# Kernel optimization log

Measured on AMD Instinct MI355X. Metric: run time of the kernel, lower is better.

Reference implementation:

```python
import jax, jax.numpy as jnp
import numpy as np

EPS = 1e-8
B, L, D = 8, 2048, 128

def _l2norm(x):
    # F.normalize-style: x / max(||x||, eps)
    n = jnp.sqrt(jnp.sum(x * x, axis=-1, keepdims=True))
    return x / jnp.maximum(n, EPS)

def setup_inputs() -> dict:
    key = jax.random.key(0)
    k0, k1, k2, k3, k4 = jax.random.split(key, 5)
    context = jax.random.normal(k0, (B, 2, L, D), dtype=jnp.float32)
    # MlpModule (BLINK-style): Linear(D, D) -> ReLU -> Linear(D, 1)
    W1 = jax.random.normal(k1, (D, D), dtype=jnp.float32) * (1.0 / np.sqrt(D))
    b1 = jnp.zeros((D,), dtype=jnp.float32)
    W2 = jax.random.normal(k2, (D, 1), dtype=jnp.float32) * (1.0 / np.sqrt(D))
    b2 = jnp.zeros((1,), dtype=jnp.float32)
    return {"context": context, "W1": W1, "b1": b1, "W2": W2, "b2": b2}

def reference(context, W1, b1, W2, b2):
    ctx = context[:, 0]          # [B, L, D] mention-side tokens
    ent = context[:, 1]          # [B, L, D] entity-side tokens
    cn = _l2norm(ctx)
    en = _l2norm(ent)
    # cosine similarity matrix [B, L, L]
    sim = jnp.einsum("bld,bmd->blm", cn, en)
    idx = jnp.argmax(sim, axis=-1)                          # [B, L]
    matched = jnp.take_along_axis(en, idx[..., None], axis=1)  # [B, L, D]
    pair = jnp.stack([cn, matched], axis=-2)                # [B, L, 2, D]
    h = jax.nn.relu(pair @ W1 + b1)                         # [B, L, 2, D]
    out = h @ W2 + b2                                       # [B, L, 2, 1]
    return jnp.sum(out, axis=-2).squeeze(-1)                # [B, L]
```

## Files before the change

### kernel.cpp

```cpp
#include <hip/hip_runtime.h>
#include <hip/hip_bf16.h>

#define B_ 8
#define L_ 2048
#define D_ 128
#define BL_ (B_ * L_)
#define DELTA2 0.016f
#define QCAP 4096

typedef __attribute__((ext_vector_type(8))) short bf16x8;
typedef __attribute__((ext_vector_type(4))) float f32x4;

__device__ __forceinline__ void gload_lds16(const void* g, void* l) {
    __builtin_amdgcn_global_load_lds(
        (const __attribute__((address_space(1))) unsigned int*)g,
        (__attribute__((address_space(3))) unsigned int*)l, 16, 0, 0);
}

#define WAIT_VM(N) asm volatile("s_waitcnt vmcnt(" #N ")" ::: "memory")

__global__ void k_norm(const float* __restrict__ ctx,
                       float* __restrict__ cn, float* __restrict__ en,
                       ushort* __restrict__ cnb, ushort* __restrict__ enb) {
    int wid  = blockIdx.x * 4 + (threadIdx.x >> 6);
    int lane = threadIdx.x & 63;
    int b   = wid >> 12;
    int rem = wid & 4095;
    int c   = rem >> 11;
    int l   = rem & 2047;

    const float* src = ctx + (size_t)wid * D_;
    float2 v = ((const float2*)src)[lane];
    float ss = v.x * v.x + v.y * v.y;
    #pragma unroll
    for (int off = 32; off; off >>= 1) ss += __shfl_down(ss, off, 64);
    ss = __shfl(ss, 0, 64);
    float n = fmaxf(sqrtf(ss), 1e-8f);
    float ox = v.x / n, oy = v.y / n;

    size_t ro = (size_t)(b * L_ + l) * D_;
    float* dst = (c == 0 ? cn : en) + ro;
    ((float2*)dst)[lane] = make_float2(ox, oy);

    __hip_bfloat16 hx = __float2bfloat16(ox), hy = __float2bfloat16(oy);
    ushort ux = *(ushort*)&hx, uy = *(ushort*)&hy;
    ushort* dstb = (c == 0 ? cnb : enb) + ro;
    ((ushort2*)dstb)[lane] = make_ushort2(ux, uy);
}

__global__ __launch_bounds__(512, 2) void k_sim(const ushort* __restrict__ cnb,
                                                const ushort* __restrict__ enb,
                                                const float* __restrict__ cn,
                                                const float* __restrict__ en,
                                                int* __restrict__ finalidx) {
    __shared__ __align__(16) char Bsm[8][4][4096];
    __shared__ float wrowmax[8][64];
    __shared__ float rowth_l[64];
    __shared__ unsigned long long best[64];
    __shared__ int qbuf[QCAP];
    __shared__ int qn;

    const int bid = blockIdx.x;
    const int b = bid & 7, rb = bid >> 3;
    const int row0 = rb * 64;
    const int tid = threadIdx.x;
    const int wave = tid >> 6, lane = tid & 63;
    const int m = lane & 15, q = lane >> 4;

    if (tid == 0) qn = 0;
    if (tid < 64) best[tid] = 0ULL;

    const ushort* Ab = cnb + ((size_t)(b * L_) + row0) * D_;
    const char* gw = (const char*)(enb + (size_t)(b * L_) * D_) + (size_t)wave * 65536;
    char* Bw = &Bsm[wave][0][0];

    bf16x8 Areg[16];
    #pragma unroll
    for (int rt = 0; rt < 4; ++rt)
        #pragma unroll
        for (int kc = 0; kc < 4; ++kc)
            Areg[rt * 4 + kc] = *(const bf16x8*)(Ab + (size_t)(rt * 16 + m) * D_ + kc * 32 + q * 8);

    auto STAGE = [&](int c) {
        const char* gc = gw + (size_t)c * 4096;
        char* lbuf = Bw + (c & 3) * 4096;
        #pragma unroll
        for (int i = 0; i < 4; ++i) {
            int j = i * 4 + q;
            int so = j * 256 + ((m ^ (j & 7)) << 4);
            gload_lds16(gc + so, lbuf + i * 1024);
        }
    };
    auto TILE = [&](int c, f32x4 acc[4]) {
        const char* lbuf = Bw + (c & 3) * 4096;
        #pragma unroll
        for (int rt = 0; rt < 4; ++rt) acc[rt] = (f32x4){0.f, 0.f, 0.f, 0.f};
        #pragma unroll
        for (int kc = 0; kc < 4; ++kc) {
            bf16x8 bf = *(const bf16x8*)(lbuf + m * 256 + ((kc * 64 + q * 16) ^ ((m & 7) << 4)));
            #pragma unroll
            for (int rt = 0; rt < 4; ++rt)
                acc[rt] = __builtin_amdgcn_mfma_f32_16x16x32_bf16(Areg[rt * 4 + kc], bf, acc[rt], 0, 0, 0);
        }
    };

    float runmax[16];
    #pragma unroll
    for (int s = 0; s < 16; ++s) runmax[s] = -3.0e38f;

    auto FMAX = [&](const f32x4 acc[4]) {
        #pragma unroll
        for (int rt = 0; rt < 4; ++rt)
            #pragma unroll
            for (int reg = 0; reg < 4; ++reg)
                runmax[rt * 4 + reg] = fmaxf(runmax[rt * 4 + reg], acc[rt][reg]);
    };

    STAGE(0); STAGE(1); STAGE(2);
    #pragma unroll 1
    for (int c = 0; c < 14; ++c) {
        WAIT_VM(8);
        f32x4 acc[4];
        TILE(c, acc);
        if (c < 13) STAGE(c + 3);
        FMAX(acc);
    }
    { WAIT_VM(4); f32x4 acc[4]; TILE(14, acc); FMAX(acc); }
    { WAIT_VM(0); f32x4 acc[4]; TILE(15, acc); FMAX(acc); }

    #pragma unroll
    for (int s = 0; s < 16; ++s) {
        float v = runmax[s];
        v = fmaxf(v, __shfl_xor(v, 1, 64));
        v = fmaxf(v, __shfl_xor(v, 2, 64));
        v = fmaxf(v, __shfl_xor(v, 4, 64));
        v = fmaxf(v, __shfl_xor(v, 8, 64));
        runmax[s] = v;
    }
    if (m == 0) {
        #pragma unroll
        for (int rt = 0; rt < 4; ++rt)
            #pragma unroll
            for (int reg = 0; reg < 4; ++reg)
                wrowmax[wave][rt * 16 + q * 4 + reg] = runmax[rt * 4 + reg];
    }
    __syncthreads();
    if (tid < 64) {
        float rm = wrowmax[0][tid];
        #pragma unroll
        for (int w = 1; w < 8; ++w) rm = fmaxf(rm, wrowmax[w][tid]);
        rowth_l[tid] = rm - DELTA2;
    }
    __syncthreads();
    float rowth_r[16];
    #pragma unroll
    for (int rt = 0; rt < 4; ++rt)
        #pragma unroll
        for (int reg = 0; reg < 4; ++reg)
            rowth_r[rt * 4 + reg] = rowth_l[rt * 16 + q * 4 + reg];

    auto CAPT = [&](int c, const f32x4 acc[4]) {
        int col = wave * 256 + c * 16 + m;
        #pragma unroll
        for (int rt = 0; rt < 4; ++rt)
            #pragma unroll
            for (int reg = 0; reg < 4; ++reg)
                if (acc[rt][reg] >= rowth_r[rt * 4 + reg]) {
                    int row = rt * 16 + q * 4 + reg;
                    int pos = atomicAdd(&qn, 1);
                    if (pos < QCAP) qbuf[pos] = (row << 12) | col;
                }
    };

    #pragma unroll 1
    for (int d = 0; d < 4; ++d) {
        f32x4 acc[4];
        TILE(15 - d, acc);
        STAGE(11 - d);
        CAPT(15 - d, acc);
    }
    #pragma unroll 1
    for (int d = 4; d < 13; ++d) {
        WAIT_VM(12);
        f32x4 acc[4];
        TILE(15 - d, acc);
        if (d < 12) STAGE(11 - d);
        CAPT(15 - d, acc);
    }
    { WAIT_VM(8); f32x4 acc[4]; TILE(2, acc); CAPT(2, acc); }
    { WAIT_VM(4); f32x4 acc[4]; TILE(1, acc); CAPT(1, acc); }
    { WAIT_VM(0); f32x4 acc[4]; TILE(0, acc); CAPT(0, acc); }
    __syncthreads();

    int qtot = min(qn, QCAP);
    for (int e0 = wave * 4; e0 < qtot; e0 += 32) {
        int e = e0 + q;
        bool act = (e < qtot);
        int pc = qbuf[act ? e : (qtot - 1)];
        int rl = (pc >> 12) & 63, col = pc & 0xFFF;
        const float* ar = cn + ((size_t)(b * L_) + row0 + rl) * D_;
        const float* br = en + ((size_t)(b * L_) + col) * D_;
        float4 x0 = ((const float4*)ar)[m * 2], x1 = ((const float4*)ar)[m * 2 + 1];
        float4 y0 = ((const float4*)br)[m * 2], y1 = ((const float4*)br)[m * 2 + 1];
        double s = (double)x0.x * y0.x + (double)x0.y * y0.y +
                   (double)x0.z * y0.z + (double)x0.w * y0.w +
                   (double)x1.x * y1.x + (double)x1.y * y1.y +
                   (double)x1.z * y1.z + (double)x1.w * y1.w;
        s += __shfl_xor(s, 1, 64);
        s += __shfl_xor(s, 2, 64);
        s += __shfl_xor(s, 4, 64);
        s += __shfl_xor(s, 8, 64);
        if (act && m == 0) {
            unsigned long long ub = (unsigned long long)__double_as_longlong(s);
            ub = (ub & 0x8000000000000000ULL) ? ~ub : (ub | 0x8000000000000000ULL);
            ub = (ub & ~0x7FFULL) | (unsigned long long)(2047 - col);
            atomicMax(&best[rl], ub);
        }
    }
    __syncthreads();
    if (tid < 64)
        finalidx[b * L_ + row0 + tid] = 2047 - (int)(best[tid] & 0x7FFULL);
}

__global__ __launch_bounds__(512) void k_mlp(
        const float* __restrict__ cn, const float* __restrict__ en,
        const int* __restrict__ finalidx,
        const float* __restrict__ W1, const float* __restrict__ b1,
        const float* __restrict__ W2, const float* __restrict__ b2,
        float* __restrict__ out) {
    __shared__ __align__(16) float As[32][68];
    __shared__ __align__(16) float Bs[32][132];
    __shared__ float redv[2][32][16];
    __shared__ int fidxs[32];

    int tid = threadIdx.x;
    int tx = tid & 15, ty = tid >> 4;
    int rr = tid >> 3, kg = tid & 7;
    int R0 = blockIdx.x * 32;
    int b  = R0 >> 11;
    int l0 = R0 & 2047;

    if (tid < 32) fidxs[tid] = finalidx[R0 + tid];

    const float* cnr = cn + ((size_t)(b * L_) + l0) * D_;
    const float* enr = en + (size_t)(b * L_) * D_;

    float acc[2][8];
    #pragma unroll
    for (int i = 0; i < 2; ++i)
        #pragma unroll
        for (int j = 0; j < 8; ++j) acc[i][j] = 0.0f;

    for (int kc = 0; kc < 4; ++kc) {
        __syncthreads();
        {
            const float* srow = (rr < 32) ? (cnr + (size_t)rr * D_)
                                          : (enr + (size_t)fidxs[rr - 32] * D_);
            float4 v = *(const float4*)(srow + kc * 32 + kg * 4);
            As[kg][rr]      = v.x;
            As[8 + kg][rr]  = v.y;
            As[16 + kg][rr] = v.z;
            As[24 + kg][rr] = v.w;
        }
        {
            int kr = tid >> 4;
            int phys = (kr & 3) * 8 + (kr >> 2);
            const float* srcp = W1 + (size_t)(kc * 32 + kr) * D_ + tx * 8;
            *(float4*)&Bs[phys][tx * 8]     = *(const float4*)(srcp);
            *(float4*)&Bs[phys][tx * 8 + 4] = *(const float4*)(srcp + 4);
        }
        __syncthreads();
        #pragma unroll
        for (int k = 0; k < 32; ++k) {
            float a0 = As[k][ty];
            float a1 = As[k][32 + ty];
            float bb[8];
            *(float4*)&bb[0] = *(const float4*)&Bs[k][tx * 4];
            *(float4*)&bb[4] = *(const float4*)&Bs[k][64 + tx * 4];
            #pragma unroll
            for (int j = 0; j < 8; ++j) {
                acc[0][j] = fmaf(a0, bb[j], acc[0][j]);
                acc[1][j] = fmaf(a1, bb[j], acc[1][j]);
            }
        }
    }

    float w2j[8], b1j[8];
    #pragma unroll
    for (int jj = 0; jj < 8; ++jj) {
        int c = (jj < 4) ? (tx * 4 + jj) : (64 + tx * 4 + (jj - 4));
        w2j[jj] = W2[c];
        b1j[jj] = b1[c];
    }
    float bias2 = b2[0];
    __syncthreads();
    #pragma unroll
    for (int i = 0; i < 2; ++i) {
        float s = 0.0f;
        #pragma unroll
        for (int jj = 0; jj < 8; ++jj)
            s += fmaxf(acc[i][jj] + b1j[jj], 0.0f) * w2j[jj];
        redv[i][ty][tx] = s;
    }
    __syncthreads();
    if (tid < 32) {
        float s0 = 0.0f, s1 = 0.0f;
        #pragma unroll
        for (int tt = 0; tt < 16; ++tt) { s0 += redv[0][tid][tt]; s1 += redv[1][tid][tt]; }
        out[R0 + tid] = (s0 + bias2) + (s1 + bias2);
    }
}

extern "C" void kernel_launch(void* const* d_in, const int* in_sizes, int n_in,
                              void* d_out, int out_size, void* d_ws, size_t ws_size,
                              hipStream_t stream) {
    const float* context = (const float*)d_in[0];
    const float* W1 = (const float*)d_in[1];
    const float* b1 = (const float*)d_in[2];
    const float* W2 = (const float*)d_in[3];
    const float* b2 = (const float*)d_in[4];
    float* out = (float*)d_out;

    char* ws = (char*)d_ws;
    float*  cn  = (float*)(ws);
    float*  en  = (float*)(ws + 8388608);
    ushort* cnb = (ushort*)(ws + 16777216);
    ushort* enb = (ushort*)(ws + 20971520);
    int* finalidx = (int*)(ws + 25165824);

    k_norm<<<8192, 256, 0, stream>>>(context, cn, en, cnb, enb);
    k_sim<<<256, 512, 0, stream>>>(cnb, enb, cn, en, finalidx);
    k_mlp<<<512, 512, 0, stream>>>(cn, en, finalidx, W1, b1, W2, b2, out);
}
```

Baseline: 125.2 us.

## Split similarity into two 256x512 tiled kernels with global atomic row-max

The fused similarity kernel is replaced by two kernels over 256-row by 512-column tiles, where all waves share one LDS ring of entity rows instead of each wave streaming its own column slice. The first kernel computes per-row maxima and merges them across column blocks with global atomicMax. The second recomputes the tile, keeps candidates above the threshold, rescores them in fp64 and resolves the argmax with global atomics. The intent is more B-operand reuse per LDS load and per-block barrier synchronisation. The cost is a second pass over the bf16 GEMM, global atomic traffic, and zeroing the buffers in the norm kernel.

```diff
diff --git a/kernel.cpp b/kernel.cpp
--- a/kernel.cpp
+++ b/kernel.cpp
@@ -21,7 +21,12 @@
 
 __global__ void k_norm(const float* __restrict__ ctx,
                        float* __restrict__ cn, float* __restrict__ en,
-                       ushort* __restrict__ cnb, ushort* __restrict__ enb) {
+                       ushort* __restrict__ cnb, ushort* __restrict__ enb,
+                       unsigned* __restrict__ rowmaxg,
+                       unsigned long long* __restrict__ bestg) {
+    int gtid = blockIdx.x * 256 + threadIdx.x;
+    if (gtid < BL_) { rowmaxg[gtid] = 0u; bestg[gtid] = 0ULL; }
+
     int wid  = blockIdx.x * 4 + (threadIdx.x >> 6);
     int lane = threadIdx.x & 63;
     int b   = wid >> 12;
@@ -48,88 +53,84 @@
     ((ushort2*)dstb)[lane] = make_ushort2(ux, uy);
 }
 
-__global__ __launch_bounds__(512, 2) void k_sim(const ushort* __restrict__ cnb,
-                                                const ushort* __restrict__ enb,
-                                                const float* __restrict__ cn,
-                                                const float* __restrict__ en,
-                                                int* __restrict__ finalidx) {
-    __shared__ __align__(16) char Bsm[8][4][4096];
-    __shared__ float wrowmax[8][64];
-    __shared__ float rowth_l[64];
-    __shared__ unsigned long long best[64];
-    __shared__ int qbuf[QCAP];
-    __shared__ int qn;
+
+#define SIM_TILE(LBUF, ACC)                                                               \
+    {                                                                                     \
+        _Pragma("unroll")                                                                 \
+        for (int rt = 0; rt < 2; ++rt)                                                    \
+            _Pragma("unroll")                                                             \
+            for (int ct = 0; ct < 2; ++ct) ACC[rt][ct] = (f32x4){0.f, 0.f, 0.f, 0.f};     \
+        _Pragma("unroll")                                                                 \
+        for (int kc = 0; kc < 4; ++kc) {                                                  \
+            int off = (kc * 64 + q * 16) ^ ((m & 7) << 4);                                \
+            bf16x8 bf0 = *(const bf16x8*)(LBUF + m * 256 + off);                          \
+            bf16x8 bf1 = *(const bf16x8*)(LBUF + (16 + m) * 256 + off);                   \
+            _Pragma("unroll")                                                             \
+            for (int rt = 0; rt < 2; ++rt) {                                              \
+                ACC[rt][0] = __builtin_amdgcn_mfma_f32_16x16x32_bf16(Areg[rt*4+kc], bf0, ACC[rt][0], 0,0,0); \
+                ACC[rt][1] = __builtin_amdgcn_mfma_f32_16x16x32_bf16(Areg[rt*4+kc], bf1, ACC[rt][1], 0,0,0); \
+            }                                                                             \
+        }                                                                                 \
+    }
+
+__global__ __launch_bounds__(512, 2) void k_sim1(const ushort* __restrict__ cnb,
+                                                 const ushort* __restrict__ enb,
+                                                 unsigned* __restrict__ rowmaxg) {
+    __shared__ __align__(16) char ring[4][8192];
 
     const int bid = blockIdx.x;
-    const int b = bid & 7, rb = bid >> 3;
-    const int row0 = rb * 64;
+    const int b = bid & 7, rem = bid >> 3;
+    const int row0 = (rem >> 2) * 256;
+    const int col0 = (rem & 3) * 512;
     const int tid = threadIdx.x;
     const int wave = tid >> 6, lane = tid & 63;
     const int m = lane & 15, q = lane >> 4;
 
-    if (tid == 0) qn = 0;
-    if (tid < 64) best[tid] = 0ULL;
-
-    const ushort* Ab = cnb + ((size_t)(b * L_) + row0) * D_;
-    const char* gw = (const char*)(enb + (size_t)(b * L_) * D_) + (size_t)wave * 65536;
-    char* Bw = &Bsm[wave][0][0];
-
-    bf16x8 Areg[16];
-    #pragma unroll
-    for (int rt = 0; rt < 4; ++rt)
+    const ushort* Ab = cnb + ((size_t)(b * L_) + row0 + wave * 32) * D_;
+    const char*   gB = (const char*)(enb + ((size_t)(b * L_) + col0) * D_);
+
+    bf16x8 Areg[8];
+    #pragma unroll
+    for (int rt = 0; rt < 2; ++rt)
         #pragma unroll
         for (int kc = 0; kc < 4; ++kc)
             Areg[rt * 4 + kc] = *(const bf16x8*)(Ab + (size_t)(rt * 16 + m) * D_ + kc * 32 + q * 8);
 
     auto STAGE = [&](int c) {
-        const char* gc = gw + (size_t)c * 4096;
-        char* lbuf = Bw + (c & 3) * 4096;
-        #pragma unroll
-        for (int i = 0; i < 4; ++i) {
-            int j = i * 4 + q;
-            int so = j * 256 + ((m ^ (j & 7)) << 4);
-            gload_lds16(gc + so, lbuf + i * 1024);
-        }
+        int j = wave * 4 + q;
+        const char* src = gB + (size_t)c * 8192 + j * 256 + ((m ^ (j & 7)) << 4);
+        gload_lds16(src, &ring[c & 3][wave * 1024]);
     };
-    auto TILE = [&](int c, f32x4 acc[4]) {
-        const char* lbuf = Bw + (c & 3) * 4096;
-        #pragma unroll
-        for (int rt = 0; rt < 4; ++rt) acc[rt] = (f32x4){0.f, 0.f, 0.f, 0.f};
-        #pragma unroll
-        for (int kc = 0; kc < 4; ++kc) {
-            bf16x8 bf = *(const bf16x8*)(lbuf + m * 256 + ((kc * 64 + q * 16) ^ ((m & 7) << 4)));
-            #pragma unroll
-            for (int rt = 0; rt < 4; ++rt)
-                acc[rt] = __builtin_amdgcn_mfma_f32_16x16x32_bf16(Areg[rt * 4 + kc], bf, acc[rt], 0, 0, 0);
-        }
-    };
-
-    float runmax[16];
-    #pragma unroll
-    for (int s = 0; s < 16; ++s) runmax[s] = -3.0e38f;
-
-    auto FMAX = [&](const f32x4 acc[4]) {
-        #pragma unroll
-        for (int rt = 0; rt < 4; ++rt)
+
+    float runmax[8];
+    #pragma unroll
+    for (int s = 0; s < 8; ++s) runmax[s] = -3.0e38f;
+
+    STAGE(0); STAGE(1); STAGE(2);
+    WAIT_VM(2);
+    __builtin_amdgcn_s_barrier();
+    #pragma unroll 1
+    for (int c = 0; c < 16; ++c) {
+        if (c < 13) STAGE(c + 3);
+        f32x4 acc[2][2];
+        const char* lbuf = ring[c & 3];
+        SIM_TILE(lbuf, acc);
+        #pragma unroll
+        for (int rt = 0; rt < 2; ++rt)
             #pragma unroll
             for (int reg = 0; reg < 4; ++reg)
-                runmax[rt * 4 + reg] = fmaxf(runmax[rt * 4 + reg], acc[rt][reg]);
-    };
-
-    STAGE(0); STAGE(1); STAGE(2);
-    #pragma unroll 1
-    for (int c = 0; c < 14; ++c) {
-        WAIT_VM(8);
-        f32x4 acc[4];
-        TILE(c, acc);
-        if (c < 13) STAGE(c + 3);
-        FMAX(acc);
-    }
-    { WAIT_VM(4); f32x4 acc[4]; TILE(14, acc); FMAX(acc); }
-    { WAIT_VM(0); f32x4 acc[4]; TILE(15, acc); FMAX(acc); }
-
-    #pragma unroll
-    for (int s = 0; s < 16; ++s) {
+                runmax[rt * 4 + reg] = fmaxf(runmax[rt * 4 + reg],
+                                             fmaxf(acc[rt][0][reg], acc[rt][1][reg]));
+        if (c < 15) {
+            if (c < 13)       WAIT_VM(2);
+            else if (c == 13) WAIT_VM(1);
+            else              WAIT_VM(0);
+            __builtin_amdgcn_s_barrier();
+        }
+    }
+
+    #pragma unroll
+    for (int s = 0; s < 8; ++s) {
         float v = runmax[s];
         v = fmaxf(v, __shfl_xor(v, 1, 64));
         v = fmaxf(v, __shfl_xor(v, 2, 64));
@@ -139,57 +140,100 @@
     }
     if (m == 0) {
         #pragma unroll
-        for (int rt = 0; rt < 4; ++rt)
+        for (int rt = 0; rt < 2; ++rt)
             #pragma unroll
-            for (int reg = 0; reg < 4; ++reg)
-                wrowmax[wave][rt * 16 + q * 4 + reg] = runmax[rt * 4 + reg];
+            for (int reg = 0; reg < 4; ++reg) {
+                int grow = b * L_ + row0 + wave * 32 + rt * 16 + q * 4 + reg;
+                unsigned u = __float_as_uint(runmax[rt * 4 + reg]);
+                u = (u & 0x80000000u) ? ~u : (u | 0x80000000u);
+                atomicMax(&rowmaxg[grow], u);
+            }
+    }
+}
+
+__global__ __launch_bounds__(512, 2) void k_sim2(const ushort* __restrict__ cnb,
+                                                 const ushort* __restrict__ enb,
+                                                 const float* __restrict__ cn,
+                                                 const float* __restrict__ en,
+                                                 const unsigned* __restrict__ rowmaxg,
+                                                 unsigned long long* __restrict__ bestg) {
+    __shared__ __align__(16) char ring[4][8192];
+    __shared__ float rowth_l[256];
+    __shared__ int qbuf[QCAP];
+    __shared__ int qn;
+
+    const int bid = blockIdx.x;
+    const int b = bid & 7, rem = bid >> 3;
+    const int row0 = (rem >> 2) * 256;
+    const int col0 = (rem & 3) * 512;
+    const int tid = threadIdx.x;
+    const int wave = tid >> 6, lane = tid & 63;
+    const int m = lane & 15, q = lane >> 4;
+
+    if (tid == 0) qn = 0;
+    if (tid < 256) {
+        unsigned u = rowmaxg[b * L_ + row0 + tid];
+        float f = (u & 0x80000000u) ? __uint_as_float(u & 0x7FFFFFFFu)
+                                    : __uint_as_float(~u);
+        rowth_l[tid] = f - DELTA2;
     }
     __syncthreads();
-    if (tid < 64) {
-        float rm = wrowmax[0][tid];
-        #pragma unroll
-        for (int w = 1; w < 8; ++w) rm = fmaxf(rm, wrowmax[w][tid]);
-        rowth_l[tid] = rm - DELTA2;
-    }
-    __syncthreads();
-    float rowth_r[16];
-    #pragma unroll
-    for (int rt = 0; rt < 4; ++rt)
+
+    float rowth_r[8];
+    #pragma unroll
+    for (int rt = 0; rt < 2; ++rt)
         #pragma unroll
         for (int reg = 0; reg < 4; ++reg)
-            rowth_r[rt * 4 + reg] = rowth_l[rt * 16 + q * 4 + reg];
-
-    auto CAPT = [&](int c, const f32x4 acc[4]) {
-        int col = wave * 256 + c * 16 + m;
-        #pragma unroll
-        for (int rt = 0; rt < 4; ++rt)
+            rowth_r[rt * 4 + reg] = rowth_l[wave * 32 + rt * 16 + q * 4 + reg];
+
+    const ushort* Ab = cnb + ((size_t)(b * L_) + row0 + wave * 32) * D_;
+    const char*   gB = (const char*)(enb + ((size_t)(b * L_) + col0) * D_);
+
+    bf16x8 Areg[8];
+    #pragma unroll
+    for (int rt = 0; rt < 2; ++rt)
+        #pragma unroll
+        for (int kc = 0; kc < 4; ++kc)
+            Areg[rt * 4 + kc] = *(const bf16x8*)(Ab + (size_t)(rt * 16 + m) * D_ + kc * 32 + q * 8);
+
+    auto STAGE = [&](int c) {
+        int j = wave * 4 + q;
+        const char* src = gB + (size_t)c * 8192 + j * 256 + ((m ^ (j & 7)) << 4);
+        gload_lds16(src, &ring[c & 3][wave * 1024]);
+    };
+
+    STAGE(0); STAGE(1); STAGE(2);
+    WAIT_VM(2);
+    __builtin_amdgcn_s_barrier();
+    #pragma unroll 1
+    for (int c = 0; c < 16; ++c) {
+        if (c < 13) STAGE(c + 3);
+        f32x4 acc[2][2];
+        const char* lbuf = ring[c & 3];
+        SIM_TILE(lbuf, acc);
+        {
             #pragma unroll
-            for (int reg = 0; reg < 4; ++reg)
-                if (acc[rt][reg] >= rowth_r[rt * 4 + reg]) {
-                    int row = rt * 16 + q * 4 + reg;
-                    int pos = atomicAdd(&qn, 1);
-                    if (pos < QCAP) qbuf[pos] = (row << 12) | col;
+            for (int rt = 0; rt < 2; ++rt)
+                #pragma unroll
+                for (int reg = 0; reg < 4; ++reg) {
+                    float th = rowth_r[rt * 4 + reg];
+                    #pragma unroll
+                    for (int ct = 0; ct < 2; ++ct)
+                        if (acc[rt][ct][reg] >= th) {
+                            int row = wave * 32 + rt * 16 + q * 4 + reg;
+                            int col = col0 + c * 32 + ct * 16 + m;
+                            int pos = atomicAdd(&qn, 1);
+                            if (pos < QCAP) qbuf[pos] = (row << 12) | col;
+                        }
                 }
-    };
-
-    #pragma unroll 1
-    for (int d = 0; d < 4; ++d) {
-        f32x4 acc[4];
-        TILE(15 - d, acc);
-        STAGE(11 - d);
-        CAPT(15 - d, acc);
-    }
-    #pragma unroll 1
-    for (int d = 4; d < 13; ++d) {
-        WAIT_VM(12);
-        f32x4 acc[4];
-        TILE(15 - d, acc);
-        if (d < 12) STAGE(11 - d);
-        CAPT(15 - d, acc);
-    }
-    { WAIT_VM(8); f32x4 acc[4]; TILE(2, acc); CAPT(2, acc); }
-    { WAIT_VM(4); f32x4 acc[4]; TILE(1, acc); CAPT(1, acc); }
-    { WAIT_VM(0); f32x4 acc[4]; TILE(0, acc); CAPT(0, acc); }
+        }
+        if (c < 15) {
+            if (c < 13)       WAIT_VM(2);
+            else if (c == 13) WAIT_VM(1);
+            else              WAIT_VM(0);
+            __builtin_amdgcn_s_barrier();
+        }
+    }
     __syncthreads();
 
     int qtot = min(qn, QCAP);
@@ -197,7 +241,7 @@
         int e = e0 + q;
         bool act = (e < qtot);
         int pc = qbuf[act ? e : (qtot - 1)];
-        int rl = (pc >> 12) & 63, col = pc & 0xFFF;
+        int rl = (pc >> 12) & 255, col = pc & 0xFFF;
         const float* ar = cn + ((size_t)(b * L_) + row0 + rl) * D_;
         const float* br = en + ((size_t)(b * L_) + col) * D_;
         float4 x0 = ((const float4*)ar)[m * 2], x1 = ((const float4*)ar)[m * 2 + 1];
@@ -214,17 +258,14 @@
             unsigned long long ub = (unsigned long long)__double_as_longlong(s);
             ub = (ub & 0x8000000000000000ULL) ? ~ub : (ub | 0x8000000000000000ULL);
             ub = (ub & ~0x7FFULL) | (unsigned long long)(2047 - col);
-            atomicMax(&best[rl], ub);
-        }
-    }
-    __syncthreads();
-    if (tid < 64)
-        finalidx[b * L_ + row0 + tid] = 2047 - (int)(best[tid] & 0x7FFULL);
+            atomicMax(&bestg[b * L_ + row0 + rl], ub);
+        }
+    }
 }
 
 __global__ __launch_bounds__(512) void k_mlp(
         const float* __restrict__ cn, const float* __restrict__ en,
-        const int* __restrict__ finalidx,
+        const unsigned long long* __restrict__ bestg,
         const float* __restrict__ W1, const float* __restrict__ b1,
         const float* __restrict__ W2, const float* __restrict__ b2,
         float* __restrict__ out) {
@@ -240,7 +281,7 @@
     int b  = R0 >> 11;
     int l0 = R0 & 2047;
 
-    if (tid < 32) fidxs[tid] = finalidx[R0 + tid];
+    if (tid < 32) fidxs[tid] = 2047 - (int)(bestg[R0 + tid] & 0x7FFULL);
 
     const float* cnr = cn + ((size_t)(b * L_) + l0) * D_;
     const float* enr = en + (size_t)(b * L_) * D_;
@@ -326,9 +367,11 @@
     float*  en  = (float*)(ws + 8388608);
     ushort* cnb = (ushort*)(ws + 16777216);
     ushort* enb = (ushort*)(ws + 20971520);
-    int* finalidx = (int*)(ws + 25165824);
-
-    k_norm<<<8192, 256, 0, stream>>>(context, cn, en, cnb, enb);
-    k_sim<<<256, 512, 0, stream>>>(cnb, enb, cn, en, finalidx);
-    k_mlp<<<512, 512, 0, stream>>>(cn, en, finalidx, W1, b1, W2, b2, out);
-}
+    unsigned* rowmaxg = (unsigned*)(ws + 25165824);
+    unsigned long long* bestg = (unsigned long long*)(ws + 25231360);
+
+    k_norm<<<8192, 256, 0, stream>>>(context, cn, en, cnb, enb, rowmaxg, bestg);
+    k_sim1<<<256, 512, 0, stream>>>(cnb, enb, rowmaxg);
+    k_sim2<<<256, 512, 0, stream>>>(cnb, enb, cn, en, rowmaxg, bestg);
+    k_mlp<<<512, 512, 0, stream>>>(cn, en, bestg, W1, b1, W2, b2, out);
+}
```

Measured after the change: 131.2 us. +4.8%, slower.

## Fuse normalization into similarity kernel via cooperative grid sync

Applied to the files above, without the earlier changes.

Merges the L2-normalization kernel into the similarity/argmax kernel. Each of the 256 blocks first normalizes its share of rows and writes the fp32 and bf16 copies, then all blocks wait on a cooperative grid-wide barrier before the similarity phase. This removes one kernel launch and the gap between kernels. In exchange it requires a cooperative launch and a grid sync, and normalization now runs on only 256 blocks, one row per wave at a time, instead of 8192 small blocks.

```diff
diff --git a/kernel.cpp b/kernel.cpp
--- a/kernel.cpp
+++ b/kernel.cpp
@@ -1,5 +1,8 @@
 #include <hip/hip_runtime.h>
 #include <hip/hip_bf16.h>
+#include <hip/hip_cooperative_groups.h>
+
+namespace cg = cooperative_groups;
 
 #define B_ 8
 #define L_ 2048
@@ -19,40 +22,11 @@
 
 #define WAIT_VM(N) asm volatile("s_waitcnt vmcnt(" #N ")" ::: "memory")
 
-__global__ void k_norm(const float* __restrict__ ctx,
-                       float* __restrict__ cn, float* __restrict__ en,
-                       ushort* __restrict__ cnb, ushort* __restrict__ enb) {
-    int wid  = blockIdx.x * 4 + (threadIdx.x >> 6);
-    int lane = threadIdx.x & 63;
-    int b   = wid >> 12;
-    int rem = wid & 4095;
-    int c   = rem >> 11;
-    int l   = rem & 2047;
-
-    const float* src = ctx + (size_t)wid * D_;
-    float2 v = ((const float2*)src)[lane];
-    float ss = v.x * v.x + v.y * v.y;
-    #pragma unroll
-    for (int off = 32; off; off >>= 1) ss += __shfl_down(ss, off, 64);
-    ss = __shfl(ss, 0, 64);
-    float n = fmaxf(sqrtf(ss), 1e-8f);
-    float ox = v.x / n, oy = v.y / n;
-
-    size_t ro = (size_t)(b * L_ + l) * D_;
-    float* dst = (c == 0 ? cn : en) + ro;
-    ((float2*)dst)[lane] = make_float2(ox, oy);
-
-    __hip_bfloat16 hx = __float2bfloat16(ox), hy = __float2bfloat16(oy);
-    ushort ux = *(ushort*)&hx, uy = *(ushort*)&hy;
-    ushort* dstb = (c == 0 ? cnb : enb) + ro;
-    ((ushort2*)dstb)[lane] = make_ushort2(ux, uy);
-}
-
-__global__ __launch_bounds__(512, 2) void k_sim(const ushort* __restrict__ cnb,
-                                                const ushort* __restrict__ enb,
-                                                const float* __restrict__ cn,
-                                                const float* __restrict__ en,
-                                                int* __restrict__ finalidx) {
+__global__ __launch_bounds__(512, 2) void k_fused(
+        const float* __restrict__ ctx,
+        float* __restrict__ cn, float* __restrict__ en,
+        ushort* __restrict__ cnb, ushort* __restrict__ enb,
+        int* __restrict__ finalidx) {
     __shared__ __align__(16) char Bsm[8][4][4096];
     __shared__ float wrowmax[8][64];
     __shared__ float rowth_l[64];
@@ -69,6 +43,34 @@
 
     if (tid == 0) qn = 0;
     if (tid < 64) best[tid] = 0ULL;
+
+    {
+        int j0 = rb * 128 + wave * 16;
+        #pragma unroll 1
+        for (int it = 0; it < 16; ++it) {
+            int j = j0 + it;
+            int c = j >> 11, l = j & 2047;
+            const float* src = ctx + (((size_t)b * 2 + c) * L_ + l) * D_;
+            float2 v = ((const float2*)src)[lane];
+            float ss = v.x * v.x + v.y * v.y;
+            #pragma unroll
+            for (int off = 32; off; off >>= 1) ss += __shfl_down(ss, off, 64);
+            ss = __shfl(ss, 0, 64);
+            float n = fmaxf(sqrtf(ss), 1e-8f);
+            float ox = v.x / n, oy = v.y / n;
+
+            size_t ro = (size_t)(b * L_ + l) * D_;
+            float* dst = (c == 0 ? cn : en) + ro;
+            ((float2*)dst)[lane] = make_float2(ox, oy);
+
+            __hip_bfloat16 hx = __float2bfloat16(ox), hy = __float2bfloat16(oy);
+            ushort ux = *(ushort*)&hx, uy = *(ushort*)&hy;
+            ushort* dstb = (c == 0 ? cnb : enb) + ro;
+            ((ushort2*)dstb)[lane] = make_ushort2(ux, uy);
+        }
+    }
+    cg::this_grid().sync();
+    WAIT_VM(0);
 
     const ushort* Ab = cnb + ((size_t)(b * L_) + row0) * D_;
     const char* gw = (const char*)(enb + (size_t)(b * L_) * D_) + (size_t)wave * 65536;
@@ -328,7 +330,9 @@
     ushort* enb = (ushort*)(ws + 20971520);
     int* finalidx = (int*)(ws + 25165824);
 
-    k_norm<<<8192, 256, 0, stream>>>(context, cn, en, cnb, enb);
-    k_sim<<<256, 512, 0, stream>>>(cnb, enb, cn, en, finalidx);
+    void* args[] = { (void*)&context, (void*)&cn, (void*)&en,
+                     (void*)&cnb, (void*)&enb, (void*)&finalidx };
+    hipLaunchCooperativeKernel((const void*)k_fused, dim3(256), dim3(512),
+                               args, 0, stream);
     k_mlp<<<512, 512, 0, stream>>>(cn, en, finalidx, W1, b1, W2, b2, out);
 }
```

After: 174.8 us. +39.7%, slower.

## Split similarity kernel into two column-halved passes with global atomic row max

Applied to the files above, without the earlier changes.

The fused sim kernel (256 blocks, each sweeping all 2048 columns twice) becomes two kernels that each cover half the columns, giving 512 blocks. Per-row maxima and best-candidate indices are combined through global atomicMax buffers that k_norm zero-initialises. The split is meant to improve GPU occupancy and parallelism, using a smaller LDS double buffer and a smaller queue capacity so more blocks fit per CU. In exchange it adds an extra kernel launch, a second full read of the bf16 tiles, global atomics, and a higher risk of overflowing the smaller candidate queue.

```diff
diff --git a/kernel.cpp b/kernel.cpp
--- a/kernel.cpp
+++ b/kernel.cpp
@@ -6,7 +6,7 @@
 #define D_ 128
 #define BL_ (B_ * L_)
 #define DELTA2 0.016f
-#define QCAP 4096
+#define QCAP 1024
 
 typedef __attribute__((ext_vector_type(8))) short bf16x8;
 typedef __attribute__((ext_vector_type(4))) float f32x4;
@@ -21,7 +21,12 @@
 
 __global__ void k_norm(const float* __restrict__ ctx,
                        float* __restrict__ cn, float* __restrict__ en,
-                       ushort* __restrict__ cnb, ushort* __restrict__ enb) {
+                       ushort* __restrict__ cnb, ushort* __restrict__ enb,
+                       unsigned* __restrict__ rowmaxg,
+                       unsigned long long* __restrict__ bestg) {
+    int gtid = blockIdx.x * 256 + threadIdx.x;
+    if (gtid < BL_) { rowmaxg[gtid] = 0u; bestg[gtid] = 0ULL; }
+
     int wid  = blockIdx.x * 4 + (threadIdx.x >> 6);
     int lane = threadIdx.x & 63;
     int b   = wid >> 12;
@@ -48,30 +53,23 @@
     ((ushort2*)dstb)[lane] = make_ushort2(ux, uy);
 }
 
-__global__ __launch_bounds__(512, 2) void k_sim(const ushort* __restrict__ cnb,
-                                                const ushort* __restrict__ enb,
-                                                const float* __restrict__ cn,
-                                                const float* __restrict__ en,
-                                                int* __restrict__ finalidx) {
-    __shared__ __align__(16) char Bsm[8][4][4096];
+
+__global__ __launch_bounds__(512, 4) void k_sim1(const ushort* __restrict__ cnb,
+                                                 const ushort* __restrict__ enb,
+                                                 unsigned* __restrict__ rowmaxg) {
+    __shared__ __align__(16) char Bsm[8][2][4096];
     __shared__ float wrowmax[8][64];
-    __shared__ float rowth_l[64];
-    __shared__ unsigned long long best[64];
-    __shared__ int qbuf[QCAP];
-    __shared__ int qn;
 
     const int bid = blockIdx.x;
-    const int b = bid & 7, rb = bid >> 3;
-    const int row0 = rb * 64;
+    const int b = bid & 7, r = bid >> 3;
+    const int row0 = (r >> 1) * 64;
+    const int col0 = (r & 1) * 1024;
     const int tid = threadIdx.x;
     const int wave = tid >> 6, lane = tid & 63;
     const int m = lane & 15, q = lane >> 4;
 
-    if (tid == 0) qn = 0;
-    if (tid < 64) best[tid] = 0ULL;
-
     const ushort* Ab = cnb + ((size_t)(b * L_) + row0) * D_;
-    const char* gw = (const char*)(enb + (size_t)(b * L_) * D_) + (size_t)wave * 65536;
+    const char* gw = (const char*)(enb + ((size_t)(b * L_) + col0 + wave * 128) * D_);
     char* Bw = &Bsm[wave][0][0];
 
     bf16x8 Areg[16];
@@ -83,7 +81,7 @@
 
     auto STAGE = [&](int c) {
         const char* gc = gw + (size_t)c * 4096;
-        char* lbuf = Bw + (c & 3) * 4096;
+        char* lbuf = Bw + (c & 1) * 4096;
         #pragma unroll
         for (int i = 0; i < 4; ++i) {
             int j = i * 4 + q;
@@ -92,7 +90,7 @@
         }
     };
     auto TILE = [&](int c, f32x4 acc[4]) {
-        const char* lbuf = Bw + (c & 3) * 4096;
+        const char* lbuf = Bw + (c & 1) * 4096;
         #pragma unroll
         for (int rt = 0; rt < 4; ++rt) acc[rt] = (f32x4){0.f, 0.f, 0.f, 0.f};
         #pragma unroll
@@ -108,25 +106,25 @@
     #pragma unroll
     for (int s = 0; s < 16; ++s) runmax[s] = -3.0e38f;
 
-    auto FMAX = [&](const f32x4 acc[4]) {
+    STAGE(0); STAGE(1);
+    #pragma unroll 1
+    for (int c = 0; c < 7; ++c) {
+        WAIT_VM(4);
+        f32x4 acc[4];
+        TILE(c, acc);
+        if (c < 6) STAGE(c + 2);
         #pragma unroll
         for (int rt = 0; rt < 4; ++rt)
             #pragma unroll
             for (int reg = 0; reg < 4; ++reg)
                 runmax[rt * 4 + reg] = fmaxf(runmax[rt * 4 + reg], acc[rt][reg]);
-    };
-
-    STAGE(0); STAGE(1); STAGE(2);
-    #pragma unroll 1
-    for (int c = 0; c < 14; ++c) {
-        WAIT_VM(8);
-        f32x4 acc[4];
-        TILE(c, acc);
-        if (c < 13) STAGE(c + 3);
-        FMAX(acc);
-    }
-    { WAIT_VM(4); f32x4 acc[4]; TILE(14, acc); FMAX(acc); }
-    { WAIT_VM(0); f32x4 acc[4]; TILE(15, acc); FMAX(acc); }
+    }
+    { WAIT_VM(0); f32x4 acc[4]; TILE(7, acc);
+      #pragma unroll
+      for (int rt = 0; rt < 4; ++rt)
+          #pragma unroll
+          for (int reg = 0; reg < 4; ++reg)
+              runmax[rt * 4 + reg] = fmaxf(runmax[rt * 4 + reg], acc[rt][reg]); }
 
     #pragma unroll
     for (int s = 0; s < 16; ++s) {
@@ -149,9 +147,40 @@
         float rm = wrowmax[0][tid];
         #pragma unroll
         for (int w = 1; w < 8; ++w) rm = fmaxf(rm, wrowmax[w][tid]);
-        rowth_l[tid] = rm - DELTA2;
-    }
-    __syncthreads();
+        unsigned u = __float_as_uint(rm);
+        u = (u & 0x80000000u) ? ~u : (u | 0x80000000u);
+        atomicMax(&rowmaxg[b * L_ + row0 + tid], u);
+    }
+}
+
+__global__ __launch_bounds__(512, 4) void k_sim2(const ushort* __restrict__ cnb,
+                                                 const ushort* __restrict__ enb,
+                                                 const float* __restrict__ cn,
+                                                 const float* __restrict__ en,
+                                                 const unsigned* __restrict__ rowmaxg,
+                                                 unsigned long long* __restrict__ bestg) {
+    __shared__ __align__(16) char Bsm[8][2][4096];
+    __shared__ float rowth_l[64];
+    __shared__ int qbuf[QCAP];
+    __shared__ int qn;
+
+    const int bid = blockIdx.x;
+    const int b = bid & 7, r = bid >> 3;
+    const int row0 = (r >> 1) * 64;
+    const int col0 = (r & 1) * 1024;
+    const int tid = threadIdx.x;
+    const int wave = tid >> 6, lane = tid & 63;
+    const int m = lane & 15, q = lane >> 4;
+
+    if (tid == 0) qn = 0;
+    if (tid < 64) {
+        unsigned u = rowmaxg[b * L_ + row0 + tid];
+        float f = (u & 0x80000000u) ? __uint_as_float(u & 0x7FFFFFFFu)
+                                    : __uint_as_float(~u);
+        rowth_l[tid] = f - DELTA2;
+    }
+    __syncthreads();
+
     float rowth_r[16];
     #pragma unroll
     for (int rt = 0; rt < 4; ++rt)
@@ -159,8 +188,41 @@
         for (int reg = 0; reg < 4; ++reg)
             rowth_r[rt * 4 + reg] = rowth_l[rt * 16 + q * 4 + reg];
 
+    const ushort* Ab = cnb + ((size_t)(b * L_) + row0) * D_;
+    const char* gw = (const char*)(enb + ((size_t)(b * L_) + col0 + wave * 128) * D_);
+    char* Bw = &Bsm[wave][0][0];
+
+    bf16x8 Areg[16];
+    #pragma unroll
+    for (int rt = 0; rt < 4; ++rt)
+        #pragma unroll
+        for (int kc = 0; kc < 4; ++kc)
+            Areg[rt * 4 + kc] = *(const bf16x8*)(Ab + (size_t)(rt * 16 + m) * D_ + kc * 32 + q * 8);
+
+    auto STAGE = [&](int c) {
+        const char* gc = gw + (size_t)c * 4096;
+        char* lbuf = Bw + (c & 1) * 4096;
+        #pragma unroll
+        for (int i = 0; i < 4; ++i) {
+            int j = i * 4 + q;
+            int so = j * 256 + ((m ^ (j & 7)) << 4);
+            gload_lds16(gc + so, lbuf + i * 1024);
+        }
+    };
+    auto TILE = [&](int c, f32x4 acc[4]) {
+        const char* lbuf = Bw + (c & 1) * 4096;
+        #pragma unroll
+        for (int rt = 0; rt < 4; ++rt) acc[rt] = (f32x4){0.f, 0.f, 0.f, 0.f};
+        #pragma unroll
+        for (int kc = 0; kc < 4; ++kc) {
+            bf16x8 bf = *(const bf16x8*)(lbuf + m * 256 + ((kc * 64 + q * 16) ^ ((m & 7) << 4)));
+            #pragma unroll
+            for (int rt = 0; rt < 4; ++rt)
+                acc[rt] = __builtin_amdgcn_mfma_f32_16x16x32_bf16(Areg[rt * 4 + kc], bf, acc[rt], 0, 0, 0);
+        }
+    };
     auto CAPT = [&](int c, const f32x4 acc[4]) {
-        int col = wave * 256 + c * 16 + m;
+        int col = col0 + wave * 128 + c * 16 + m;
         #pragma unroll
         for (int rt = 0; rt < 4; ++rt)
             #pragma unroll
@@ -172,24 +234,16 @@
                 }
     };
 
+    STAGE(0); STAGE(1);
     #pragma unroll 1
-    for (int d = 0; d < 4; ++d) {
+    for (int c = 0; c < 7; ++c) {
+        WAIT_VM(4);
         f32x4 acc[4];
-        TILE(15 - d, acc);
-        STAGE(11 - d);
-        CAPT(15 - d, acc);
-    }
-    #pragma unroll 1
-    for (int d = 4; d < 13; ++d) {
-        WAIT_VM(12);
-        f32x4 acc[4];
-        TILE(15 - d, acc);
-        if (d < 12) STAGE(11 - d);
-        CAPT(15 - d, acc);
-    }
-    { WAIT_VM(8); f32x4 acc[4]; TILE(2, acc); CAPT(2, acc); }
-    { WAIT_VM(4); f32x4 acc[4]; TILE(1, acc); CAPT(1, acc); }
-    { WAIT_VM(0); f32x4 acc[4]; TILE(0, acc); CAPT(0, acc); }
+        TILE(c, acc);
+        if (c < 6) STAGE(c + 2);
+        CAPT(c, acc);
+    }
+    { WAIT_VM(0); f32x4 acc[4]; TILE(7, acc); CAPT(7, acc); }
     __syncthreads();
 
     int qtot = min(qn, QCAP);
@@ -214,17 +268,14 @@
             unsigned long long ub = (unsigned long long)__double_as_longlong(s);
             ub = (ub & 0x8000000000000000ULL) ? ~ub : (ub | 0x8000000000000000ULL);
             ub = (ub & ~0x7FFULL) | (unsigned long long)(2047 - col);
-            atomicMax(&best[rl], ub);
-        }
-    }
-    __syncthreads();
-    if (tid < 64)
-        finalidx[b * L_ + row0 + tid] = 2047 - (int)(best[tid] & 0x7FFULL);
+            atomicMax(&bestg[b * L_ + row0 + rl], ub);
+        }
+    }
 }
 
 __global__ __launch_bounds__(512) void k_mlp(
         const float* __restrict__ cn, const float* __restrict__ en,
-        const int* __restrict__ finalidx,
+        const unsigned long long* __restrict__ bestg,
         const float* __restrict__ W1, const float* __restrict__ b1,
         const float* __restrict__ W2, const float* __restrict__ b2,
         float* __restrict__ out) {
@@ -240,7 +291,7 @@
     int b  = R0 >> 11;
     int l0 = R0 & 2047;
 
-    if (tid < 32) fidxs[tid] = finalidx[R0 + tid];
+    if (tid < 32) fidxs[tid] = 2047 - (int)(bestg[R0 + tid] & 0x7FFULL);
 
     const float* cnr = cn + ((size_t)(b * L_) + l0) * D_;
     const float* enr = en + (size_t)(b * L_) * D_;
@@ -326,9 +377,11 @@
     float*  en  = (float*)(ws + 8388608);
     ushort* cnb = (ushort*)(ws + 16777216);
     ushort* enb = (ushort*)(ws + 20971520);
-    int* finalidx = (int*)(ws + 25165824);
-
-    k_norm<<<8192, 256, 0, stream>>>(context, cn, en, cnb, enb);
-    k_sim<<<256, 512, 0, stream>>>(cnb, enb, cn, en, finalidx);
-    k_mlp<<<512, 512, 0, stream>>>(cn, en, finalidx, W1, b1, W2, b2, out);
-}
+    unsigned* rowmaxg = (unsigned*)(ws + 25165824);
+    unsigned long long* bestg = (unsigned long long*)(ws + 25231360);
+
+    k_norm<<<8192, 256, 0, stream>>>(context, cn, en, cnb, enb, rowmaxg, bestg);
+    k_sim1<<<512, 512, 0, stream>>>(cnb, enb, rowmaxg);
+    k_sim2<<<512, 512, 0, stream>>>(cnb, enb, cn, en, rowmaxg, bestg);
+    k_mlp<<<512, 512, 0, stream>>>(cn, en, bestg, W1, b1, W2, b2, out);
+}
```

Result: slower. 134.4 us (+7.4%).
